# Kernel tuning notes

Measured on AMD Instinct MI355X. Metric: run time of the kernel, lower is better.

Reference implementation:

```python
import jax, jax.numpy as jnp
import numpy as np
import math

K = 8       # wavelet order (k)
C = 8       # channels (c)
ALPHA = 64  # retained Fourier modes
L = 0       # coarsest level
B = 32
N = 8192    # power of two


def setup_inputs() -> dict:
    key = jax.random.key(0)
    ks = jax.random.split(key, 14)
    ck = C * K
    scale = 1.0 / (ck * ck)  # matches torch: 1/(c*k)**2
    f32 = jnp.float32
    inp = {
        "x": jax.random.normal(ks[0], (B, N, C, K), dtype=f32),
        # SparseKernelFT1d weights (complex, stored as re/im): scale * rand
        "wA_re": scale * jax.random.uniform(ks[1], (ck, ck, ALPHA), dtype=f32),
        "wA_im": scale * jax.random.uniform(ks[2], (ck, ck, ALPHA), dtype=f32),
        "wB_re": scale * jax.random.uniform(ks[3], (ck, ck, ALPHA), dtype=f32),
        "wB_im": scale * jax.random.uniform(ks[4], (ck, ck, ALPHA), dtype=f32),
        "wC_re": scale * jax.random.uniform(ks[5], (ck, ck, ALPHA), dtype=f32),
        "wC_im": scale * jax.random.uniform(ks[6], (ck, ck, ALPHA), dtype=f32),
        # T0 linear layer (k -> k)
        "T0_w": jax.random.normal(ks[7], (K, K), dtype=f32) / math.sqrt(K),
        "T0_b": 0.01 * jax.random.normal(ks[8], (K,), dtype=f32),
        # Legendre wavelet filter buffers: ec_* are [H0.T;H1.T] / [G0.T;G1.T] (2k,k),
        # rc_* are [H0;G0] / [H1;G1] (2k,k). Stand-ins: random orthonormal-ish matrices
        # scaled like wavelet filters (same math regardless of exact values).
        "ec_s": jax.random.normal(ks[9], (2 * K, K), dtype=f32) / math.sqrt(2 * K),
        "ec_d": jax.random.normal(ks[10], (2 * K, K), dtype=f32) / math.sqrt(2 * K),
        "rc_e": jax.random.normal(ks[11], (2 * K, K), dtype=f32) / math.sqrt(2 * K),
        "rc_o": jax.random.normal(ks[12], (2 * K, K), dtype=f32) / math.sqrt(2 * K),
    }
    return inp


def _sparse_ft(x, w_re, w_im):
    # x: [B, N, c, k] -> spectral mixing over first ALPHA rfft modes
    Bb, Nn, c, k = x.shape
    xv = x.reshape(Bb, Nn, c * k).transpose(0, 2, 1)   # [B, ck, N]
    xf = jnp.fft.rfft(xv)                               # [B, ck, N//2+1] complex
    l = min(ALPHA, Nn // 2 + 1)
    W = (w_re[:, :, :l] + 1j * w_im[:, :, :l]).astype(jnp.complex64)
    of = jnp.einsum('bix,iox->box', xf[:, :, :l], W)
    out_ft = jnp.zeros((Bb, c * k, Nn // 2 + 1), dtype=jnp.complex64).at[:, :, :l].set(of)
    xo = jnp.fft.irfft(out_ft, n=Nn)                    # [B, ck, N] real
    return xo.transpose(0, 2, 1).reshape(Bb, Nn, c, k)


def reference(x, wA_re, wA_im, wB_re, wB_im, wC_re, wC_im, T0_w, T0_b,
              ec_s, ec_d, rc_e, rc_o):
    Bb, Nn, c, k = x.shape
    ns = int(math.floor(math.log2(Nn)))
    Ud, Us = [], []
    # --- decomposition ---
    for _ in range(ns - L):
        xa = jnp.concatenate([x[:, ::2], x[:, 1::2]], axis=-1)  # [B, N/2, c, 2k]
        d = xa @ ec_d                                           # [B, N/2, c, k]
        s = xa @ ec_s
        Ud.append(_sparse_ft(d, wA_re, wA_im) + _sparse_ft(s, wB_re, wB_im))
        Us.append(_sparse_ft(d, wC_re, wC_im))
        x = s
    # --- coarsest-level linear ---
    x = x @ T0_w.T + T0_b
    # --- reconstruction (u_s is None branch) ---
    for i in range(ns - 1 - L, -1, -1):
        x = x + Us[i]
        xc = jnp.concatenate([x, Ud[i]], axis=-1)               # [B, n, c, 2k]
        x_e = xc @ rc_e
        x_o = xc @ rc_o
        Bc, Nc, cc, _ = xc.shape
        x = jnp.stack([x_e, x_o], axis=2).reshape(Bc, Nc * 2, cc, K)  # interleave even/odd
    return (x,) + tuple(Ud) + tuple(Us)
```

## Files before the change

kernel.cpp:

```cpp
#include <hip/hip_runtime.h>

#define BB 32
#define CKD 64
#define CC 8
#define KK 8
#define FPW 132

__device__ const int D_FCB[14] = {0,8,12,14,15,16,17,18,19,20,21,22,23,24};
__device__ const int D_RP[14] = {0,32,48,56,60,62,63,64,65,66,67,68,69,70};
__device__ const int D_KBS[13] = {128,64,32,16,8,4,2,1,1,1,1,1,1};
__device__ const int D_PVP[13] = {0,128,192,224,240,248,252,254,255,256,257,258,259};
__device__ const int D_TB[14] = {0,64,96,112,120,124,126,127,128,129,130,131,132,133};
__device__ const int D_L[13]  = {64,64,64,64,64,64,33,17,9,5,3,2,1};
__device__ const int D_FTOF[13] = {0,524288,786432,917504,983040,1015808,1032192,
                                   1048576,1064960,1081344,1097728,1114112,1130496};
__device__ const int D_XP[65] = {0,13,25,36,46,56,65,74,83,92,100,108,116,124,132,140,
    148,156,163,170,177,184,191,198,205,212,219,226,233,240,247,254,261,268,274,280,
    286,292,298,304,310,316,322,328,334,340,346,352,358,364,370,376,382,388,394,400,
    406,412,418,424,430,436,442,448,454};

typedef __attribute__((ext_vector_type(4))) short s4v;
typedef __attribute__((ext_vector_type(8))) short s8v;
typedef __attribute__((ext_vector_type(4))) float f4v;

static __device__ __forceinline__ float4 ld4(const float* p){ return *(const float4*)p; }
static __device__ __forceinline__ size_t d_udo(int i){ return 33554432ull - (16777216u >> i); }
static __device__ __forceinline__ size_t d_uso(int i){ return 50329600ull - (16777216u >> i); }
static __device__ __forceinline__ size_t d_tof(int i){ return 128ull * (8192u - (8192u >> i)); }

static __device__ __forceinline__ unsigned short b16(float f) {
    unsigned u = __float_as_uint(f);
    u += 0x7FFFu + ((u >> 16) & 1u);
    return (unsigned short)(u >> 16);
}
static __device__ __forceinline__ float fb16(unsigned short h) {
    return __uint_as_float(((unsigned)h) << 16);
}

__global__ __launch_bounds__(256) void gen_tbl2_k(unsigned short* __restrict__ Th,
        unsigned short* __restrict__ Tl, unsigned short* __restrict__ Tfh,
        unsigned short* __restrict__ Tfl) {
    int lvl = blockIdx.y;
    int nh = 4096 >> lvl;
    int idx = blockIdx.x * 256 + threadIdx.x;
    if (blockIdx.z == 0) {
        if (idx >= nh * 128) return;
        int t = idx >> 7, k = idx & 127, x = k >> 1;
        int l = nh / 2 + 1; if (l > 64) l = 64;
        float v = 0.f;
        if (x < l) {
            int r = (x * t) & (nh - 1);
            float th = 6.283185307179586f * ((float)r / (float)nh);
            float s, c; sincosf(th, &s, &c);
            v = (k & 1) ? s : c;
        }
        unsigned short hi = b16(v);
        unsigned short lo = b16(v - fb16(hi));
        size_t off = d_tof(lvl) + idx;
        Th[off] = hi; Tl[off] = lo;
    } else {
        int nhp = nh < 128 ? 128 : nh;
        if (idx >= 128 * nhp) return;
        int j = idx & 7;
        int lane = (idx >> 3) & 63;
        int mt = (idx >> 9) & 7;
        int kb = idx >> 12;
        int row = mt*16 + (lane & 15);
        int t = kb*32 + (lane >> 4)*8 + j;
        int x = row >> 1;
        int l = nh / 2 + 1; if (l > 64) l = 64;
        float v = 0.f;
        if (x < l && t < nh) {
            int r = (x * t) & (nh - 1);
            float th = 6.283185307179586f * ((float)r / (float)nh);
            float s, c; sincosf(th, &s, &c);
            v = (row & 1) ? -s : c;
        }
        unsigned short hi = b16(v);
        unsigned short lo = b16(v - fb16(hi));
        size_t off = (size_t)D_FTOF[lvl] + idx;
        Tfh[off] = hi; Tfl[off] = lo;
    }
}

__global__ __launch_bounds__(256) void wtr_k(const float* __restrict__ wAr,
        const float* __restrict__ wAi, const float* __restrict__ wBr,
        const float* __restrict__ wBi, const float* __restrict__ wCr,
        const float* __restrict__ wCi, float* __restrict__ wt) {
    int x = blockIdx.x, arr = blockIdx.y;
    const float* W;
    switch (arr) {
        case 0: W = wAr; break;
        case 1: W = wAi; break;
        case 2: W = wBr; break;
        case 3: W = wBi; break;
        case 4: W = wCr; break;
        default: W = wCi; break;
    }
    float* o = wt + ((size_t)arr*64 + x)*4096;
    for (int q = threadIdx.x; q < 4096; q += 256)
        o[q] = W[(size_t)q*64 + x];
}

__global__ __launch_bounds__(256) void wbig_k(const float* __restrict__ wt,
        unsigned short* __restrict__ wbh, unsigned short* __restrict__ wbl) {
    int x = blockIdx.x;
    int f0 = blockIdx.y * 2048;
    for (int q = threadIdx.x; q < 2048; q += 256) {
        int f = f0 + q;
        int j = f & 7;
        int lane = (f >> 3) & 63;
        int nt = (f >> 9) & 15;
        int kt = f >> 13;
        int k = kt*32 + (lane >> 4)*8 + j;
        int n = nt*16 + (lane & 15);
        int pk = k >> 6, i = k & 63;
        int pn = n >> 6, o = n & 63;
        int arr; float sgn;
        switch ((pn << 2) | pk) {
            case 0:  arr = 0; sgn =  1.f; break;
            case 1:  arr = 1; sgn = -1.f; break;
            case 2:  arr = 2; sgn =  1.f; break;
            case 3:  arr = 3; sgn = -1.f; break;
            case 4:  arr = 1; sgn = -1.f; break;
            case 5:  arr = 0; sgn = -1.f; break;
            case 6:  arr = 3; sgn = -1.f; break;
            case 7:  arr = 2; sgn = -1.f; break;
            case 8:  arr = 4; sgn =  1.f; break;
            case 9:  arr = 5; sgn = -1.f; break;
            case 12: arr = 5; sgn = -1.f; break;
            case 13: arr = 4; sgn = -1.f; break;
            default: arr = -1; sgn = 0.f; break;
        }
        float v = 0.f;
        if (arr >= 0) v = sgn * wt[((size_t)arr*64 + x)*4096 + (size_t)i*64 + o];
        unsigned short h = b16(v);
        unsigned short l2 = b16(v - fb16(h));
        wbh[(size_t)x*65536 + f] = h;
        wbl[(size_t)x*65536 + f] = l2;
    }
}

__global__ __launch_bounds__(256) void decomp_k(const float* __restrict__ xin,
        const float* __restrict__ ecd, const float* __restrict__ ecs,
        float* __restrict__ dslot, float* __restrict__ sslot, int nh) {
    int idx = blockIdx.x * 256 + threadIdx.x;
    if (idx >= BB * nh * CC) return;
    int c = idx & 7;
    int t = (idx >> 3) % nh;
    int b = idx / (nh * CC);
    const float* p0 = xin + ((size_t)b * 2 * nh + 2 * t) * CKD + c * KK;
    float xa[16];
    float4 v;
    v = ld4(p0);      xa[0]=v.x; xa[1]=v.y; xa[2]=v.z; xa[3]=v.w;
    v = ld4(p0+4);    xa[4]=v.x; xa[5]=v.y; xa[6]=v.z; xa[7]=v.w;
    v = ld4(p0+64);   xa[8]=v.x; xa[9]=v.y; xa[10]=v.z; xa[11]=v.w;
    v = ld4(p0+68);   xa[12]=v.x; xa[13]=v.y; xa[14]=v.z; xa[15]=v.w;
    float dd[8], ss[8];
    #pragma unroll
    for (int m = 0; m < 8; m++) { dd[m] = 0.f; ss[m] = 0.f; }
    #pragma unroll
    for (int j = 0; j < 16; j++) {
        float xv = xa[j];
        #pragma unroll
        for (int m = 0; m < 8; m++) {
            dd[m] = fmaf(xv, ecd[j*8+m], dd[m]);
            ss[m] = fmaf(xv, ecs[j*8+m], ss[m]);
        }
    }
    size_t ob = ((size_t)b * nh + t) * CKD + c * KK;
    *(float4*)(dslot+ob)   = make_float4(dd[0],dd[1],dd[2],dd[3]);
    *(float4*)(dslot+ob+4) = make_float4(dd[4],dd[5],dd[6],dd[7]);
    *(float4*)(sslot+ob)   = make_float4(ss[0],ss[1],ss[2],ss[3]);
    *(float4*)(sslot+ob+4) = make_float4(ss[4],ss[5],ss[6],ss[7]);
}

__global__ __launch_bounds__(256) void decomp_small_k(const float* __restrict__ s4base,
        const float* __restrict__ ecd, const float* __restrict__ ecs,
        const float* __restrict__ T0w, const float* __restrict__ T0b,
        float* __restrict__ outbuf, float* __restrict__ xt0) {
    __shared__ float sA[128*64];
    __shared__ float sB[64*64];
    int b = blockIdx.x, tid = threadIdx.x;
    for (int lvl = 5; lvl <= 12; lvl++) {
        int nh = 4096 >> lvl;
        const float* src = (lvl == 5) ? (s4base + (size_t)b*256*CKD)
                                      : (((lvl - 6) & 1) ? sB : sA);
        float* dst = ((lvl - 5) & 1) ? sB : sA;
        float* dG = outbuf + d_udo(lvl) + (size_t)b*nh*CKD;
        float* sG = outbuf + d_uso(lvl) + (size_t)b*nh*CKD;
        for (int q = tid; q < nh*8; q += 256) {
            int c = q & 7, t = q >> 3;
            const float* p0 = src + (size_t)(2*t)*CKD + c*KK;
            float xa[16];
            float4 v;
            v = ld4(p0);      xa[0]=v.x; xa[1]=v.y; xa[2]=v.z; xa[3]=v.w;
            v = ld4(p0+4);    xa[4]=v.x; xa[5]=v.y; xa[6]=v.z; xa[7]=v.w;
            v = ld4(p0+64);   xa[8]=v.x; xa[9]=v.y; xa[10]=v.z; xa[11]=v.w;
            v = ld4(p0+68);   xa[12]=v.x; xa[13]=v.y; xa[14]=v.z; xa[15]=v.w;
            float dd[8], ss[8];
            #pragma unroll
            for (int m = 0; m < 8; m++) { dd[m] = 0.f; ss[m] = 0.f; }
            #pragma unroll
            for (int j = 0; j < 16; j++) {
                float xv = xa[j];
                #pragma unroll
                for (int m = 0; m < 8; m++) {
                    dd[m] = fmaf(xv, ecd[j*8+m], dd[m]);
                    ss[m] = fmaf(xv, ecs[j*8+m], ss[m]);
                }
            }
            size_t ob = (size_t)t * CKD + c * KK;
            *(float4*)(dG+ob)   = make_float4(dd[0],dd[1],dd[2],dd[3]);
            *(float4*)(dG+ob+4) = make_float4(dd[4],dd[5],dd[6],dd[7]);
            *(float4*)(sG+ob)   = make_float4(ss[0],ss[1],ss[2],ss[3]);
            *(float4*)(sG+ob+4) = make_float4(ss[4],ss[5],ss[6],ss[7]);
            float* dl = dst + t*CKD + c*KK;
            #pragma unroll
            for (int j = 0; j < 8; j++) dl[j] = ss[j];
        }
        __syncthreads();
    }
    if (tid < 64) {
        int m = tid & 7, c = tid >> 3;
        const float* xr = sB + c*KK;
        float a = T0b[m];
        #pragma unroll
        for (int j = 0; j < 8; j++) a = fmaf(xr[j], T0w[m*8+j], a);
        xt0[(size_t)b*64 + tid] = a;
    }
}

__global__ __launch_bounds__(256) void repack_k(const float* __restrict__ outbuf,
        unsigned* __restrict__ pv) {
    __shared__ unsigned vp[64*FPW];
    int slot = blockIdx.x;
    int lvl = 0;
    while (lvl < 12 && slot >= D_RP[lvl+1]) lvl++;
    int nh = 4096 >> lvl;
    int c = slot - D_RP[lvl];
    int t0s = c * 128;
    int kbs = D_KBS[lvl];
    int b = blockIdx.y, z = blockIdx.z;
    const float* V = outbuf + (z ? d_uso(lvl) : d_udo(lvl)) + (size_t)b * nh * CKD;
    int tid = threadIdx.x;
    #pragma unroll
    for (int q = 0; q < 8; q++) {
        int fi = tid + 256*q;
        int tl_ = fi >> 4;
        int t = t0s + tl_;
        int i4 = (fi & 15) * 4;
        float4 v = make_float4(0.f,0.f,0.f,0.f);
        if (t < nh) v = ld4(V + (size_t)t*CKD + i4);
        const float* pvv = &v.x;
        #pragma unroll
        for (int j = 0; j < 4; j++) {
            int row = i4 + j;
            float f = pvv[j];
            unsigned u = __float_as_uint(f);
            unsigned hi = u & 0xFFFF0000u;
            float r = f - __uint_as_float(hi);
            unsigned lo = __float_as_uint(r) & 0xFFFF0000u;
            int cw = tl_ ^ (((row >> 3) & 7) << 2);
            vp[row*FPW + cw] = (hi >> 16) | lo;
        }
    }
    __syncthreads();
    unsigned* P = pv + (size_t)D_PVP[lvl]*131072 + (size_t)b*kbs*4096;
    #pragma unroll
    for (int q = 0; q < 8; q++) {
        int fi = tid + 256*q;
        int j4 = fi & 1;
        int lane2 = (fi >> 1) & 63;
        int nt = (fi >> 7) & 3;
        int kbl = fi >> 9;
        int kbg = c*4 + kbl;
        if (kbg >= kbs) continue;
        int lrow = nt*16 + (lane2 & 15);
        int cb = kbl*32 + (lane2 >> 4)*8 + j4*4;
        int rsw = ((lrow >> 3) & 7) << 2;
        uint4 v = *(const uint4*)&vp[lrow*FPW + (cb ^ rsw)];
        *(uint4*)(P + (((size_t)(kbg*8 + z*4 + nt))*64 + lane2)*8 + j4*4) = v;
    }
}

__global__ __launch_bounds__(256) void fft_fwd_mfma_k(const unsigned* __restrict__ pv,
        const unsigned short* __restrict__ Tfh, const unsigned short* __restrict__ Tfl,
        float* __restrict__ xfpf, float2* __restrict__ xf_all) {
    int slot = blockIdx.x;
    int lvl = 0;
    while (lvl < 12 && slot >= D_FCB[lvl+1]) lvl++;
    int kbs = D_KBS[lvl];
    int nslots = D_FCB[lvl+1] - D_FCB[lvl];
    int kb0 = (slot - D_FCB[lvl]) * 16;
    int kb1 = kb0 + 16; if (kb1 > kbs) kb1 = kbs;
    int b = blockIdx.y;
    const unsigned* PV = pv + (size_t)D_PVP[lvl]*131072 + (size_t)b*kbs*4096;
    const unsigned short* THb = Tfh + D_FTOF[lvl];
    const unsigned short* TLb = Tfl + D_FTOF[lvl];
    int tid = threadIdx.x;
    int w = tid >> 6, lane = tid & 63;
    int col = lane & 15, khi = lane >> 4;
    int mt0 = w * 2;
    f4v acc[2][8];
    #pragma unroll
    for (int m = 0; m < 2; m++)
        #pragma unroll
        for (int n = 0; n < 8; n++) acc[m][n] = (f4v){0.f,0.f,0.f,0.f};
    for (int kb = kb0; kb < kb1; kb++) {
        s8v ah[2], al[2];
        #pragma unroll
        for (int m = 0; m < 2; m++) {
            size_t fo = (((size_t)kb*8 + (mt0 + m))*64 + lane)*8;
            ah[m] = *(const s8v*)(THb + fo);
            al[m] = *(const s8v*)(TLb + fo);
        }
        #pragma unroll
        for (int n = 0; n < 8; n++) {
            const unsigned* bp = PV + (((size_t)(kb*8 + n))*64 + lane)*8;
            uint4 w0 = *(const uint4*)bp;
            uint4 w1 = *(const uint4*)(bp + 4);
            s8v bh, bl;
            const unsigned* pw = &w0.x;
            #pragma unroll
            for (int j = 0; j < 4; j++) {
                bh[j] = (short)(pw[j] & 0xFFFFu);
                bl[j] = (short)(pw[j] >> 16);
            }
            pw = &w1.x;
            #pragma unroll
            for (int j = 0; j < 4; j++) {
                bh[4+j] = (short)(pw[j] & 0xFFFFu);
                bl[4+j] = (short)(pw[j] >> 16);
            }
            #pragma unroll
            for (int m = 0; m < 2; m++) {
                acc[m][n] = __builtin_amdgcn_mfma_f32_16x16x32_bf16(ah[m], bh, acc[m][n], 0,0,0);
                acc[m][n] = __builtin_amdgcn_mfma_f32_16x16x32_bf16(ah[m], bl, acc[m][n], 0,0,0);
                acc[m][n] = __builtin_amdgcn_mfma_f32_16x16x32_bf16(al[m], bh, acc[m][n], 0,0,0);
            }
        }
    }
    if (nslots == 1) {
        float* XB = (float*)xf_all + (size_t)lvl*524288 + (size_t)b*16384;
        #pragma unroll
        for (int m = 0; m < 2; m++) {
            int m0 = (mt0 + m)*16 + khi*4;
            #pragma unroll
            for (int n = 0; n < 8; n++) {
                int ic = n*16 + col;
                int z = ic >> 6, i = ic & 63;
                float* X = XB + (size_t)z*8192;
                #pragma unroll
                for (int r = 0; r < 4; r++) {
                    int row = m0 + r;
                    X[(((size_t)(row >> 1)*64 + i) << 1) | (row & 1)] = acc[m][n][r];
                }
            }
        }
    } else {
        #pragma unroll
        for (int m = 0; m < 2; m++) {
            int m0 = (mt0 + m)*16 + khi*4;
            #pragma unroll
            for (int n = 0; n < 8; n++) {
                int ic = n*16 + col;
                int z = ic >> 6, i = ic & 63;
                float* P = xfpf + ((size_t)slot*64 + (size_t)b*2 + z) * 8192;
                #pragma unroll
                for (int r = 0; r < 4; r++)
                    P[(size_t)(m0 + r)*64 + i] = acc[m][n][r];
            }
        }
    }
}

__global__ __launch_bounds__(256) void reduce_fwd_k(const float* __restrict__ xfpf,
        float2* __restrict__ xf_all) {
    int lvl = blockIdx.y;
    int e = blockIdx.x * 256 + threadIdx.x;
    int j = e & 4095;
    int bz = e >> 12;
    int x = j >> 6, i = j & 63;
    int c0 = D_FCB[lvl], c1 = D_FCB[lvl+1];
    float re = 0.f, im = 0.f;
    for (int c = c0; c < c1; c++) {
        size_t base = ((size_t)c*64 + bz) * 8192;
        re += xfpf[base + (size_t)(2*x)*64 + i];
        im += xfpf[base + (size_t)(2*x+1)*64 + i];
    }
    xf_all[(size_t)lvl*262144 + (size_t)bz*4096 + j] = make_float2(re, im);
}

__global__ __launch_bounds__(256) void mix_mfma_k(const float2* __restrict__ xf_all,
        const unsigned short* __restrict__ wbh, const unsigned short* __restrict__ wbl,
        unsigned* __restrict__ ofp) {
    __shared__ unsigned ax[32*260];
    int x = 0;
    while (x < 64 && (int)blockIdx.x >= D_XP[x+1]) x++;
    int lvl = blockIdx.x - D_XP[x];
    int nh = 4096 >> lvl;
    const float2* xfL = xf_all + (size_t)lvl*262144;
    int tid = threadIdx.x;
    for (int q = tid; q < 4096; q += 256) {
        int b = q >> 7, z = (q >> 6) & 1, i = q & 63;
        float2 v = xfL[((size_t)b*2 + z)*4096 + (size_t)x*64 + i];
        int sw = ((b >> 3) & 7) << 2;
        int kR = z*128 + i;
        unsigned uR = __float_as_uint(v.x);
        unsigned hiR = uR & 0xFFFF0000u;
        float rR = v.x - __uint_as_float(hiR);
        unsigned loR = __float_as_uint(rR) & 0xFFFF0000u;
        ax[b*260 + (kR ^ sw)] = (hiR >> 16) | loR;
        unsigned uI = __float_as_uint(v.y);
        unsigned hiI = uI & 0xFFFF0000u;
        float rI = v.y - __uint_as_float(hiI);
        unsigned loI = __float_as_uint(rI) & 0xFFFF0000u;
        ax[b*260 + ((kR + 64) ^ sw)] = (hiI >> 16) | loI;
    }
    __syncthreads();
    int w4 = tid >> 6, lane = tid & 63;
    int col = lane & 15, khi = lane >> 4;
    int mt = w4 & 1, nt0 = (w4 >> 1) * 8;
    int arow = mt*16 + col;
    int asw = ((arow >> 3) & 7) << 2;
    const unsigned* ap = ax + arow*260;
    const unsigned short* WBH = wbh + (size_t)x*65536;
    const unsigned short* WBL = wbl + (size_t)x*65536;
    f4v acc[8];
    #pragma unroll
    for (int n = 0; n < 8; n++) acc[n] = (f4v){0.f,0.f,0.f,0.f};
    #pragma unroll
    for (int kt = 0; kt < 8; kt++) {
        int cb = kt*32 + khi*8;
        uint4 a0 = *(const uint4*)(ap + (cb ^ asw));
        uint4 a1 = *(const uint4*)(ap + ((cb + 4) ^ asw));
        s8v ah, al;
        const unsigned* pw = &a0.x;
        #pragma unroll
        for (int j = 0; j < 4; j++) {
            ah[j] = (short)(pw[j] & 0xFFFFu);
            al[j] = (short)(pw[j] >> 16);
        }
        pw = &a1.x;
        #pragma unroll
        for (int j = 0; j < 4; j++) {
            ah[4+j] = (short)(pw[j] & 0xFFFFu);
            al[4+j] = (short)(pw[j] >> 16);
        }
        #pragma unroll
        for (int n = 0; n < 8; n++) {
            int nt = nt0 + n;
            size_t fo = (((size_t)kt*16 + nt)*64 + lane)*8;
            s8v bh = *(const s8v*)(WBH + fo);
            s8v bl = *(const s8v*)(WBL + fo);
            acc[n] = __builtin_amdgcn_mfma_f32_16x16x32_bf16(ah, bh, acc[n], 0, 0, 0);
            acc[n] = __builtin_amdgcn_mfma_f32_16x16x32_bf16(ah, bl, acc[n], 0, 0, 0);
            acc[n] = __builtin_amdgcn_mfma_f32_16x16x32_bf16(al, bh, acc[n], 0, 0, 0);
        }
    }
    float wfac = (x == 0 || 2*x == nh) ? 1.f : 2.f;
    float sc = wfac / (float)nh;
    int k0 = 2*x;
    #pragma unroll
    for (int n = 0; n < 8; n++) {
        int nn = nt0 + n;
        int pn = nn >> 2;
        int o = (nn & 3)*16 + col;
        int z = pn >> 1;
        int kr = k0 + (pn & 1);
        #pragma unroll
        for (int r = 0; r < 4; r++) {
            int b = mt*16 + khi*4 + r;
            size_t base = (((size_t)lvl*32 + b)*2 + z)*8192 + (size_t)kr*64 + o;
            float v = sc * acc[n][r];
            unsigned short h = b16(v);
            unsigned short l2 = b16(v - fb16(h));
            ofp[base] = (unsigned)h | ((unsigned)l2 << 16);
        }
    }
}

__global__ __launch_bounds__(256) void fft_inv_mfma_k(
        const unsigned* __restrict__ ofp,
        const unsigned short* __restrict__ Th,  const unsigned short* __restrict__ Tl,
        float* __restrict__ outbuf) {
    __shared__ unsigned gp[2*64*132];
    int lvl = 0;
    while (lvl < 12 && (int)blockIdx.x >= D_TB[lvl+1]) lvl++;
    int g = blockIdx.x - D_TB[lvl];
    int nh = 4096 >> lvl;
    int tbase = g * 64;
    int b = blockIdx.y;
    int tid = threadIdx.x;
    const unsigned* Gp = ofp + (((size_t)lvl*32 + b)*2)*8192;
    #pragma unroll
    for (int q = 0; q < 16; q++) {
        int fi = tid + 256*q;
        int z = fi >> 11;
        int rem = fi & 2047;
        int k = rem >> 4, o4 = (rem & 15)*4;
        uint4 v = *(const uint4*)(Gp + (size_t)z*8192 + (size_t)k*64 + o4);
        const unsigned* pw = &v.x;
        #pragma unroll
        for (int i = 0; i < 4; i++)
            gp[z*8448 + (o4+i)*132 + k] = pw[i];
    }
    __syncthreads();
    int w = tid >> 6;
    int lane = tid & 63;
    int tb = tbase + w*16;
    if (tb >= nh) return;
    int trow = lane & 15, khi = lane >> 4;
    int tA = tb + trow; if (tA >= nh) tA = nh - 1;
    const unsigned short* THp = Th + d_tof(lvl) + (size_t)tA*128 + khi*8;
    const unsigned short* TLp = Tl + d_tof(lvl) + (size_t)tA*128 + khi*8;
    f4v acc[8];
    #pragma unroll
    for (int n = 0; n < 8; n++) acc[n] = (f4v){0.f,0.f,0.f,0.f};
    #pragma unroll
    for (int kk = 0; kk < 4; kk++) {
        s8v ah = *(const s8v*)(THp + kk*32);
        s8v al = *(const s8v*)(TLp + kk*32);
        #pragma unroll
        for (int n = 0; n < 8; n++) {
            int z = n >> 2;
            int off = z*8448 + ((n & 3)*16 + trow)*132 + kk*32 + khi*8;
            uint4 w0 = *(const uint4*)(gp + off);
            uint4 w1 = *(const uint4*)(gp + off + 4);
            s8v bh, bl;
            const unsigned* pw = &w0.x;
            #pragma unroll
            for (int j = 0; j < 4; j++) {
                bh[j] = (short)(pw[j] & 0xFFFFu);
                bl[j] = (short)(pw[j] >> 16);
            }
            pw = &w1.x;
            #pragma unroll
            for (int j = 0; j < 4; j++) {
                bh[4+j] = (short)(pw[j] & 0xFFFFu);
                bl[4+j] = (short)(pw[j] >> 16);
            }
            acc[n] = __builtin_amdgcn_mfma_f32_16x16x32_bf16(ah, bh, acc[n], 0, 0, 0);
            acc[n] = __builtin_amdgcn_mfma_f32_16x16x32_bf16(ah, bl, acc[n], 0, 0, 0);
            acc[n] = __builtin_amdgcn_mfma_f32_16x16x32_bf16(al, bh, acc[n], 0, 0, 0);
        }
    }
    float* U0 = outbuf + d_udo(lvl) + (size_t)b * nh * CKD;
    float* U1 = outbuf + d_uso(lvl) + (size_t)b * nh * CKD;
    int thi4 = khi * 4;
    #pragma unroll
    for (int n = 0; n < 8; n++) {
        float* U = (n >> 2) ? U1 : U0;
        int ocol = (n & 3)*16 + trow;
        #pragma unroll
        for (int r = 0; r < 4; r++) {
            int t = tb + thi4 + r;
            if (t < nh) U[(size_t)t*64 + ocol] = acc[n][r];
        }
    }
}

__global__ __launch_bounds__(256) void recon_small_k(const float* __restrict__ xt0,
        const float* __restrict__ outbuf,
        const float* __restrict__ rce, const float* __restrict__ rco,
        float* __restrict__ rb0) {
    __shared__ float xA[128*64];
    __shared__ float xB[64*64];
    int b = blockIdx.x, tid = threadIdx.x;
    if (tid < 64) xB[tid] = xt0[(size_t)b*64 + tid];
    __syncthreads();
    for (int i = 12; i >= 6; i--) {
        int nh = 4096 >> i;
        const float* cur = ((i == 12) || !(i & 1)) ? xB : xA;
        float* nxt = (i & 1) ? xB : xA;
        const float* Us = outbuf + d_uso(i) + (size_t)b*nh*CKD;
        const float* Ud = outbuf + d_udo(i) + (size_t)b*nh*CKD;
        for (int q = tid; q < nh*8; q += 256) {
            int c = q & 7, t = q >> 3;
            size_t base = (size_t)t*CKD + c*KK;
            float xc[16];
            float4 a0 = ld4(cur+base), a1 = ld4(cur+base+4);
            float4 u0 = ld4(Us+base),  u1 = ld4(Us+base+4);
            float4 d0 = ld4(Ud+base),  d1 = ld4(Ud+base+4);
            xc[0]=a0.x+u0.x; xc[1]=a0.y+u0.y; xc[2]=a0.z+u0.z; xc[3]=a0.w+u0.w;
            xc[4]=a1.x+u1.x; xc[5]=a1.y+u1.y; xc[6]=a1.z+u1.z; xc[7]=a1.w+u1.w;
            xc[8]=d0.x;  xc[9]=d0.y;  xc[10]=d0.z; xc[11]=d0.w;
            xc[12]=d1.x; xc[13]=d1.y; xc[14]=d1.z; xc[15]=d1.w;
            float e[8], o2[8];
            #pragma unroll
            for (int m = 0; m < 8; m++) { e[m] = 0.f; o2[m] = 0.f; }
            #pragma unroll
            for (int j = 0; j < 16; j++) {
                float xv = xc[j];
                #pragma unroll
                for (int m = 0; m < 8; m++) {
                    e[m]  = fmaf(xv, rce[j*8+m], e[m]);
                    o2[m] = fmaf(xv, rco[j*8+m], o2[m]);
                }
            }
            if (i > 6) {
                float* pe = nxt + (size_t)(2*t)*CKD + c*KK;
                #pragma unroll
                for (int j = 0; j < 8; j++) { pe[j] = e[j]; pe[CKD + j] = o2[j]; }
            } else {
                float* pe = rb0 + ((size_t)b*128 + 2*t)*CKD + c*KK;
                *(float4*)(pe)      = make_float4(e[0],e[1],e[2],e[3]);
                *(float4*)(pe+4)    = make_float4(e[4],e[5],e[6],e[7]);
                *(float4*)(pe+64)   = make_float4(o2[0],o2[1],o2[2],o2[3]);
                *(float4*)(pe+68)   = make_float4(o2[4],o2[5],o2[6],o2[7]);
            }
        }
        __syncthreads();
    }
}

__global__ __launch_bounds__(256) void recon_k(const float* __restrict__ xin,
        const float* __restrict__ us, const float* __restrict__ ud,
        const float* __restrict__ rce, const float* __restrict__ rco,
        float* __restrict__ xout, int nh) {
    int idx = blockIdx.x*256 + threadIdx.x;
    if (idx >= BB*nh*CC) return;
    int c = idx & 7;
    int t = (idx >> 3) % nh;
    int b = idx / (nh*CC);
    size_t base = ((size_t)b*nh + t)*CKD + c*KK;
    float xc[16];
    float4 a0 = ld4(xin+base), a1 = ld4(xin+base+4);
    float4 u0 = ld4(us+base),  u1 = ld4(us+base+4);
    float4 d0 = ld4(ud+base),  d1 = ld4(ud+base+4);
    xc[0]=a0.x+u0.x; xc[1]=a0.y+u0.y; xc[2]=a0.z+u0.z; xc[3]=a0.w+u0.w;
    xc[4]=a1.x+u1.x; xc[5]=a1.y+u1.y; xc[6]=a1.z+u1.z; xc[7]=a1.w+u1.w;
    xc[8]=d0.x;  xc[9]=d0.y;  xc[10]=d0.z; xc[11]=d0.w;
    xc[12]=d1.x; xc[13]=d1.y; xc[14]=d1.z; xc[15]=d1.w;
    float e[8], o2[8];
    #pragma unroll
    for (int m = 0; m < 8; m++) { e[m] = 0.f; o2[m] = 0.f; }
    #pragma unroll
    for (int j = 0; j < 16; j++) {
        float xv = xc[j];
        #pragma unroll
        for (int m = 0; m < 8; m++) {
            e[m]  = fmaf(xv, rce[j*8+m], e[m]);
            o2[m] = fmaf(xv, rco[j*8+m], o2[m]);
        }
    }
    size_t ob = ((size_t)b*2*nh + 2*t)*CKD + c*KK;
    *(float4*)(xout+ob)      = make_float4(e[0],e[1],e[2],e[3]);
    *(float4*)(xout+ob+4)    = make_float4(e[4],e[5],e[6],e[7]);
    *(float4*)(xout+ob+64)   = make_float4(o2[0],o2[1],o2[2],o2[3]);
    *(float4*)(xout+ob+68)   = make_float4(o2[4],o2[5],o2[6],o2[7]);
}

extern "C" void kernel_launch(void* const* d_in, const int* in_sizes, int n_in,
                              void* d_out, int out_size, void* d_ws, size_t ws_size,
                              hipStream_t stream) {
    const float* x   = (const float*)d_in[0];
    const float* wAr = (const float*)d_in[1];
    const float* wAi = (const float*)d_in[2];
    const float* wBr = (const float*)d_in[3];
    const float* wBi = (const float*)d_in[4];
    const float* wCr = (const float*)d_in[5];
    const float* wCi = (const float*)d_in[6];
    const float* T0w = (const float*)d_in[7];
    const float* T0b = (const float*)d_in[8];
    const float* ecs = (const float*)d_in[9];
    const float* ecd = (const float*)d_in[10];
    const float* rce = (const float*)d_in[11];
    const float* rco = (const float*)d_in[12];
    float* out = (float*)d_out;
    float* wsf = (float*)d_ws;

    size_t p = 0;
    float2* xf_all = (float2*)(wsf + p); p += 6815744;
    unsigned* ofp = (unsigned*)(wsf + p); p += 6815744;
    unsigned short* Th  = (unsigned short*)(wsf + p); p += 528384;
    unsigned short* Tl  = (unsigned short*)(wsf + p); p += 528384;
    unsigned short* Tfh = (unsigned short*)(wsf + p); p += 573440;
    unsigned short* Tfl = (unsigned short*)(wsf + p); p += 573440;
    float*  wt   = wsf + p; p += 1572864;
    unsigned short* wbh = (unsigned short*)(wsf + p); p += 2097152;
    unsigned short* wbl = (unsigned short*)(wsf + p); p += 2097152;
    float*  xt0  = wsf + p; p += 2048;
    float*  rb0  = wsf + p; p += 4194304;
    float*  rb1  = wsf + p; p += 8388608;
    float*  xfpf = wsf + p; p += 36700160;
    unsigned* pv = (unsigned*)(wsf + p); p += 34078720;
    (void)ws_size; (void)in_sizes; (void)n_in; (void)out_size;

    size_t udo[13], uso[13];
    for (int i = 0; i < 13; i++) {
        udo[i] = 33554432ull - (16777216u >> i);
        uso[i] = 50329600ull - (16777216u >> i);
    }

    gen_tbl2_k<<<dim3(2048, 13, 2), 256, 0, stream>>>(Th, Tl, Tfh, Tfl);
    wtr_k<<<dim3(64, 6), 256, 0, stream>>>(wAr, wAi, wBr, wBi, wCr, wCi, wt);
    wbig_k<<<dim3(64, 32), 256, 0, stream>>>(wt, wbh, wbl);

    for (int i = 0; i < 5; i++) {
        int nh = 4096 >> i;
        const float* xin_l = (i == 0) ? x : (out + uso[i-1]);
        int tot = BB * nh * CC;
        decomp_k<<<(tot + 255)/256, 256, 0, stream>>>(xin_l, ecd, ecs, out + udo[i], out + uso[i], nh);
    }
    decomp_small_k<<<BB, 256, 0, stream>>>(out + uso[4], ecd, ecs, T0w, T0b, out, xt0);

    repack_k<<<dim3(70, BB, 2), 256, 0, stream>>>(out, pv);
    fft_fwd_mfma_k<<<dim3(24, BB), 256, 0, stream>>>(pv, Tfh, Tfl, xfpf, xf_all);
    reduce_fwd_k<<<dim3(1024, 3), 256, 0, stream>>>(xfpf, xf_all);
    mix_mfma_k<<<454, 256, 0, stream>>>(xf_all, wbh, wbl, ofp);
    fft_inv_mfma_k<<<dim3(133, BB), 256, 0, stream>>>(ofp, Th, Tl, out);

    recon_small_k<<<BB, 256, 0, stream>>>(xt0, out, rce, rco, rb0);
    const float* rin = rb0;
    for (int i = 5; i >= 0; i--) {
        int nh = 4096 >> i;
        float* ro = (i == 0) ? out : ((i & 1) ? rb1 : rb0);
        int tot = BB * nh * CC;
        recon_k<<<(tot + 255)/256, 256, 0, stream>>>(rin, out + uso[i], out + udo[i], rce, rco, ro, nh);
        rin = ro;
    }
}
```

Before: 438.6 us.

## Fuse repack into decomposition and drop split-K forward FFT reduction

```diff
diff --git a/kernel.cpp b/kernel.cpp
--- a/kernel.cpp
+++ b/kernel.cpp
@@ -6,12 +6,9 @@
 #define KK 8
 #define FPW 132
 
-__device__ const int D_FCB[14] = {0,8,12,14,15,16,17,18,19,20,21,22,23,24};
-__device__ const int D_RP[14] = {0,32,48,56,60,62,63,64,65,66,67,68,69,70};
 __device__ const int D_KBS[13] = {128,64,32,16,8,4,2,1,1,1,1,1,1};
 __device__ const int D_PVP[13] = {0,128,192,224,240,248,252,254,255,256,257,258,259};
 __device__ const int D_TB[14] = {0,64,96,112,120,124,126,127,128,129,130,131,132,133};
-__device__ const int D_L[13]  = {64,64,64,64,64,64,33,17,9,5,3,2,1};
 __device__ const int D_FTOF[13] = {0,524288,786432,917504,983040,1015808,1032192,
                                    1048576,1064960,1081344,1097728,1114112,1130496};
 __device__ const int D_XP[65] = {0,13,25,36,46,56,65,74,83,92,100,108,116,124,132,140,
@@ -35,6 +32,13 @@
 }
 static __device__ __forceinline__ float fb16(unsigned short h) {
     return __uint_as_float(((unsigned)h) << 16);
+}
+static __device__ __forceinline__ unsigned packhl(float f) {
+    unsigned u = __float_as_uint(f);
+    unsigned hi = u & 0xFFFF0000u;
+    float r = f - __uint_as_float(hi);
+    unsigned lo = __float_as_uint(r) & 0xFFFF0000u;
+    return (hi >> 16) | lo;
 }
 
 __global__ __launch_bounds__(256) void gen_tbl2_k(unsigned short* __restrict__ Th,
@@ -143,52 +147,82 @@
 
 __global__ __launch_bounds__(256) void decomp_k(const float* __restrict__ xin,
         const float* __restrict__ ecd, const float* __restrict__ ecs,
-        float* __restrict__ dslot, float* __restrict__ sslot, int nh) {
-    int idx = blockIdx.x * 256 + threadIdx.x;
-    if (idx >= BB * nh * CC) return;
-    int c = idx & 7;
-    int t = (idx >> 3) % nh;
-    int b = idx / (nh * CC);
-    const float* p0 = xin + ((size_t)b * 2 * nh + 2 * t) * CKD + c * KK;
-    float xa[16];
-    float4 v;
-    v = ld4(p0);      xa[0]=v.x; xa[1]=v.y; xa[2]=v.z; xa[3]=v.w;
-    v = ld4(p0+4);    xa[4]=v.x; xa[5]=v.y; xa[6]=v.z; xa[7]=v.w;
-    v = ld4(p0+64);   xa[8]=v.x; xa[9]=v.y; xa[10]=v.z; xa[11]=v.w;
-    v = ld4(p0+68);   xa[12]=v.x; xa[13]=v.y; xa[14]=v.z; xa[15]=v.w;
-    float dd[8], ss[8];
-    #pragma unroll
-    for (int m = 0; m < 8; m++) { dd[m] = 0.f; ss[m] = 0.f; }
-    #pragma unroll
-    for (int j = 0; j < 16; j++) {
-        float xv = xa[j];
-        #pragma unroll
-        for (int m = 0; m < 8; m++) {
-            dd[m] = fmaf(xv, ecd[j*8+m], dd[m]);
-            ss[m] = fmaf(xv, ecs[j*8+m], ss[m]);
-        }
-    }
-    size_t ob = ((size_t)b * nh + t) * CKD + c * KK;
-    *(float4*)(dslot+ob)   = make_float4(dd[0],dd[1],dd[2],dd[3]);
-    *(float4*)(dslot+ob+4) = make_float4(dd[4],dd[5],dd[6],dd[7]);
-    *(float4*)(sslot+ob)   = make_float4(ss[0],ss[1],ss[2],ss[3]);
-    *(float4*)(sslot+ob+4) = make_float4(ss[4],ss[5],ss[6],ss[7]);
+        float* __restrict__ sslot, unsigned* __restrict__ pvL,
+        int nh, int kbs) {
+    __shared__ unsigned vd[64*FPW];
+    __shared__ unsigned vs[64*FPW];
+    int chunk = blockIdx.x, b = blockIdx.y;
+    int t0 = chunk * 128;
+    int tid = threadIdx.x;
+    #pragma unroll
+    for (int wi = 0; wi < 4; wi++) {
+        int q = tid + wi*256;
+        int c = q & 7, tl = q >> 3;
+        int t = t0 + tl;
+        const float* p0 = xin + ((size_t)b*2*nh + 2*t)*CKD + c*KK;
+        float xa[16];
+        float4 v;
+        v = ld4(p0);      xa[0]=v.x; xa[1]=v.y; xa[2]=v.z; xa[3]=v.w;
+        v = ld4(p0+4);    xa[4]=v.x; xa[5]=v.y; xa[6]=v.z; xa[7]=v.w;
+        v = ld4(p0+64);   xa[8]=v.x; xa[9]=v.y; xa[10]=v.z; xa[11]=v.w;
+        v = ld4(p0+68);   xa[12]=v.x; xa[13]=v.y; xa[14]=v.z; xa[15]=v.w;
+        float dd[8], ss[8];
+        #pragma unroll
+        for (int m = 0; m < 8; m++) { dd[m] = 0.f; ss[m] = 0.f; }
+        #pragma unroll
+        for (int j = 0; j < 16; j++) {
+            float xv = xa[j];
+            #pragma unroll
+            for (int m = 0; m < 8; m++) {
+                dd[m] = fmaf(xv, ecd[j*8+m], dd[m]);
+                ss[m] = fmaf(xv, ecs[j*8+m], ss[m]);
+            }
+        }
+        float* sp = sslot + ((size_t)b*nh + t)*CKD + c*KK;
+        *(float4*)sp     = make_float4(ss[0],ss[1],ss[2],ss[3]);
+        *(float4*)(sp+4) = make_float4(ss[4],ss[5],ss[6],ss[7]);
+        #pragma unroll
+        for (int j = 0; j < 8; j++) {
+            int row = c*8 + j;
+            int cw = tl ^ (((row >> 3) & 7) << 2);
+            vd[row*FPW + cw] = packhl(dd[j]);
+            vs[row*FPW + cw] = packhl(ss[j]);
+        }
+    }
+    __syncthreads();
+    unsigned* P = pvL + (size_t)b*kbs*4096;
+    #pragma unroll
+    for (int qq = 0; qq < 16; qq++) {
+        int fi = tid + 256*qq;
+        int z = fi >> 11;
+        int rem = fi & 2047;
+        int j4 = rem & 1;
+        int lane2 = (rem >> 1) & 63;
+        int nt = (rem >> 7) & 3;
+        int kbl = rem >> 9;
+        int kbg = chunk*4 + kbl;
+        int lrow = nt*16 + (lane2 & 15);
+        int cb = kbl*32 + (lane2 >> 4)*8 + j4*4;
+        int rsw = ((lrow >> 3) & 7) << 2;
+        const unsigned* src = z ? vs : vd;
+        uint4 v = *(const uint4*)&src[lrow*FPW + (cb ^ rsw)];
+        *(uint4*)(P + (((size_t)(kbg*8 + z*4 + nt))*64 + lane2)*8 + j4*4) = v;
+    }
 }
 
 __global__ __launch_bounds__(256) void decomp_small_k(const float* __restrict__ s4base,
         const float* __restrict__ ecd, const float* __restrict__ ecs,
         const float* __restrict__ T0w, const float* __restrict__ T0b,
-        float* __restrict__ outbuf, float* __restrict__ xt0) {
+        unsigned* __restrict__ pv, float* __restrict__ xt0) {
     __shared__ float sA[128*64];
     __shared__ float sB[64*64];
+    __shared__ unsigned sDp[128*64];
     int b = blockIdx.x, tid = threadIdx.x;
     for (int lvl = 5; lvl <= 12; lvl++) {
         int nh = 4096 >> lvl;
         const float* src = (lvl == 5) ? (s4base + (size_t)b*256*CKD)
                                       : (((lvl - 6) & 1) ? sB : sA);
         float* dst = ((lvl - 5) & 1) ? sB : sA;
-        float* dG = outbuf + d_udo(lvl) + (size_t)b*nh*CKD;
-        float* sG = outbuf + d_uso(lvl) + (size_t)b*nh*CKD;
         for (int q = tid; q < nh*8; q += 256) {
             int c = q & 7, t = q >> 3;
             const float* p0 = src + (size_t)(2*t)*CKD + c*KK;
@@ -210,14 +244,33 @@
                     ss[m] = fmaf(xv, ecs[j*8+m], ss[m]);
                 }
             }
-            size_t ob = (size_t)t * CKD + c * KK;
-            *(float4*)(dG+ob)   = make_float4(dd[0],dd[1],dd[2],dd[3]);
-            *(float4*)(dG+ob+4) = make_float4(dd[4],dd[5],dd[6],dd[7]);
-            *(float4*)(sG+ob)   = make_float4(ss[0],ss[1],ss[2],ss[3]);
-            *(float4*)(sG+ob+4) = make_float4(ss[4],ss[5],ss[6],ss[7]);
             float* dl = dst + t*CKD + c*KK;
-            #pragma unroll
-            for (int j = 0; j < 8; j++) dl[j] = ss[j];
+            unsigned* dp = sDp + t*CKD + c*KK;
+            #pragma unroll
+            for (int j = 0; j < 8; j++) {
+                dl[j] = ss[j];
+                dp[j] = packhl(dd[j]);
+            }
+        }
+        __syncthreads();
+        int kbs = D_KBS[lvl];
+        unsigned* P = pv + (size_t)D_PVP[lvl]*131072 + (size_t)b*kbs*4096;
+        for (int f = tid; f < kbs*512; f += 256) {
+            int lane = f & 63;
+            int zn = (f >> 6) & 7;
+            int kb = f >> 9;
+            int z = zn >> 2, nt = zn & 3;
+            int i = nt*16 + (lane & 15);
+            int tb2 = kb*32 + (lane >> 4)*8;
+            unsigned vals[8];
+            #pragma unroll
+            for (int j = 0; j < 8; j++) {
+                int t = tb2 + j;
+                vals[j] = z ? packhl(dst[t*CKD + i]) : sDp[t*CKD + i];
+            }
+            unsigned* pp = P + (((size_t)(kb*8 + z*4 + nt))*64 + lane)*8;
+            *(uint4*)pp     = make_uint4(vals[0],vals[1],vals[2],vals[3]);
+            *(uint4*)(pp+4) = make_uint4(vals[4],vals[5],vals[6],vals[7]);
         }
         __syncthreads();
     }
@@ -231,69 +284,11 @@
     }
 }
 
-__global__ __launch_bounds__(256) void repack_k(const float* __restrict__ outbuf,
-        unsigned* __restrict__ pv) {
-    __shared__ unsigned vp[64*FPW];
-    int slot = blockIdx.x;
-    int lvl = 0;
-    while (lvl < 12 && slot >= D_RP[lvl+1]) lvl++;
-    int nh = 4096 >> lvl;
-    int c = slot - D_RP[lvl];
-    int t0s = c * 128;
-    int kbs = D_KBS[lvl];
-    int b = blockIdx.y, z = blockIdx.z;
-    const float* V = outbuf + (z ? d_uso(lvl) : d_udo(lvl)) + (size_t)b * nh * CKD;
-    int tid = threadIdx.x;
-    #pragma unroll
-    for (int q = 0; q < 8; q++) {
-        int fi = tid + 256*q;
-        int tl_ = fi >> 4;
-        int t = t0s + tl_;
-        int i4 = (fi & 15) * 4;
-        float4 v = make_float4(0.f,0.f,0.f,0.f);
-        if (t < nh) v = ld4(V + (size_t)t*CKD + i4);
-        const float* pvv = &v.x;
-        #pragma unroll
-        for (int j = 0; j < 4; j++) {
-            int row = i4 + j;
-            float f = pvv[j];
-            unsigned u = __float_as_uint(f);
-            unsigned hi = u & 0xFFFF0000u;
-            float r = f - __uint_as_float(hi);
-            unsigned lo = __float_as_uint(r) & 0xFFFF0000u;
-            int cw = tl_ ^ (((row >> 3) & 7) << 2);
-            vp[row*FPW + cw] = (hi >> 16) | lo;
-        }
-    }
-    __syncthreads();
-    unsigned* P = pv + (size_t)D_PVP[lvl]*131072 + (size_t)b*kbs*4096;
-    #pragma unroll
-    for (int q = 0; q < 8; q++) {
-        int fi = tid + 256*q;
-        int j4 = fi & 1;
-        int lane2 = (fi >> 1) & 63;
-        int nt = (fi >> 7) & 3;
-        int kbl = fi >> 9;
-        int kbg = c*4 + kbl;
-        if (kbg >= kbs) continue;
-        int lrow = nt*16 + (lane2 & 15);
-        int cb = kbl*32 + (lane2 >> 4)*8 + j4*4;
-        int rsw = ((lrow >> 3) & 7) << 2;
-        uint4 v = *(const uint4*)&vp[lrow*FPW + (cb ^ rsw)];
-        *(uint4*)(P + (((size_t)(kbg*8 + z*4 + nt))*64 + lane2)*8 + j4*4) = v;
-    }
-}
-
 __global__ __launch_bounds__(256) void fft_fwd_mfma_k(const unsigned* __restrict__ pv,
         const unsigned short* __restrict__ Tfh, const unsigned short* __restrict__ Tfl,
-        float* __restrict__ xfpf, float2* __restrict__ xf_all) {
-    int slot = blockIdx.x;
-    int lvl = 0;
-    while (lvl < 12 && slot >= D_FCB[lvl+1]) lvl++;
+        float2* __restrict__ xf_all) {
+    int lvl = blockIdx.x;
     int kbs = D_KBS[lvl];
-    int nslots = D_FCB[lvl+1] - D_FCB[lvl];
-    int kb0 = (slot - D_FCB[lvl]) * 16;
-    int kb1 = kb0 + 16; if (kb1 > kbs) kb1 = kbs;
     int b = blockIdx.y;
     const unsigned* PV = pv + (size_t)D_PVP[lvl]*131072 + (size_t)b*kbs*4096;
     const unsigned short* THb = Tfh + D_FTOF[lvl];
@@ -307,7 +302,7 @@
     for (int m = 0; m < 2; m++)
         #pragma unroll
         for (int n = 0; n < 8; n++) acc[m][n] = (f4v){0.f,0.f,0.f,0.f};
-    for (int kb = kb0; kb < kb1; kb++) {
+    for (int kb = 0; kb < kbs; kb++) {
         s8v ah[2], al[2];
         #pragma unroll
         for (int m = 0; m < 2; m++) {
@@ -341,55 +336,22 @@
             }
         }
     }
-    if (nslots == 1) {
-        float* XB = (float*)xf_all + (size_t)lvl*524288 + (size_t)b*16384;
-        #pragma unroll
-        for (int m = 0; m < 2; m++) {
-            int m0 = (mt0 + m)*16 + khi*4;
-            #pragma unroll
-            for (int n = 0; n < 8; n++) {
-                int ic = n*16 + col;
-                int z = ic >> 6, i = ic & 63;
-                float* X = XB + (size_t)z*8192;
-                #pragma unroll
-                for (int r = 0; r < 4; r++) {
-                    int row = m0 + r;
-                    X[(((size_t)(row >> 1)*64 + i) << 1) | (row & 1)] = acc[m][n][r];
-                }
-            }
-        }
-    } else {
-        #pragma unroll
-        for (int m = 0; m < 2; m++) {
-            int m0 = (mt0 + m)*16 + khi*4;
-            #pragma unroll
-            for (int n = 0; n < 8; n++) {
-                int ic = n*16 + col;
-                int z = ic >> 6, i = ic & 63;
-                float* P = xfpf + ((size_t)slot*64 + (size_t)b*2 + z) * 8192;
-                #pragma unroll
-                for (int r = 0; r < 4; r++)
-                    P[(size_t)(m0 + r)*64 + i] = acc[m][n][r];
-            }
-        }
-    }
-}
-
-__global__ __launch_bounds__(256) void reduce_fwd_k(const float* __restrict__ xfpf,
-        float2* __restrict__ xf_all) {
-    int lvl = blockIdx.y;
-    int e = blockIdx.x * 256 + threadIdx.x;
-    int j = e & 4095;
-    int bz = e >> 12;
-    int x = j >> 6, i = j & 63;
-    int c0 = D_FCB[lvl], c1 = D_FCB[lvl+1];
-    float re = 0.f, im = 0.f;
-    for (int c = c0; c < c1; c++) {
-        size_t base = ((size_t)c*64 + bz) * 8192;
-        re += xfpf[base + (size_t)(2*x)*64 + i];
-        im += xfpf[base + (size_t)(2*x+1)*64 + i];
-    }
-    xf_all[(size_t)lvl*262144 + (size_t)bz*4096 + j] = make_float2(re, im);
+    float* XB = (float*)xf_all + (size_t)lvl*524288 + (size_t)b*16384;
+    #pragma unroll
+    for (int m = 0; m < 2; m++) {
+        int m0 = (mt0 + m)*16 + khi*4;
+        #pragma unroll
+        for (int n = 0; n < 8; n++) {
+            int ic = n*16 + col;
+            int z = ic >> 6, i = ic & 63;
+            float* X = XB + (size_t)z*8192;
+            #pragma unroll
+            for (int r = 0; r < 4; r++) {
+                int row = m0 + r;
+                X[(((size_t)(row >> 1)*64 + i) << 1) | (row & 1)] = acc[m][n][r];
+            }
+        }
+    }
 }
 
 __global__ __launch_bounds__(256) void mix_mfma_k(const float2* __restrict__ xf_all,
@@ -407,16 +369,8 @@
         float2 v = xfL[((size_t)b*2 + z)*4096 + (size_t)x*64 + i];
         int sw = ((b >> 3) & 7) << 2;
         int kR = z*128 + i;
-        unsigned uR = __float_as_uint(v.x);
-        unsigned hiR = uR & 0xFFFF0000u;
-        float rR = v.x - __uint_as_float(hiR);
-        unsigned loR = __float_as_uint(rR) & 0xFFFF0000u;
-        ax[b*260 + (kR ^ sw)] = (hiR >> 16) | loR;
-        unsigned uI = __float_as_uint(v.y);
-        unsigned hiI = uI & 0xFFFF0000u;
-        float rI = v.y - __uint_as_float(hiI);
-        unsigned loI = __float_as_uint(rI) & 0xFFFF0000u;
-        ax[b*260 + ((kR + 64) ^ sw)] = (hiI >> 16) | loI;
+        ax[b*260 + (kR ^ sw)] = packhl(v.x);
+        ax[b*260 + ((kR + 64) ^ sw)] = packhl(v.y);
     }
     __syncthreads();
     int w4 = tid >> 6, lane = tid & 63;
@@ -473,10 +427,7 @@
         for (int r = 0; r < 4; r++) {
             int b = mt*16 + khi*4 + r;
             size_t base = (((size_t)lvl*32 + b)*2 + z)*8192 + (size_t)kr*64 + o;
-            float v = sc * acc[n][r];
-            unsigned short h = b16(v);
-            unsigned short l2 = b16(v - fb16(h));
-            ofp[base] = (unsigned)h | ((unsigned)l2 << 16);
+            ofp[base] = packhl(sc * acc[n][r]);
         }
     }
 }
@@ -684,7 +635,6 @@
     float*  xt0  = wsf + p; p += 2048;
     float*  rb0  = wsf + p; p += 4194304;
     float*  rb1  = wsf + p; p += 8388608;
-    float*  xfpf = wsf + p; p += 36700160;
     unsigned* pv = (unsigned*)(wsf + p); p += 34078720;
     (void)ws_size; (void)in_sizes; (void)n_in; (void)out_size;
 
@@ -693,6 +643,8 @@
         udo[i] = 33554432ull - (16777216u >> i);
         uso[i] = 50329600ull - (16777216u >> i);
     }
+    const int kbs_h[5] = {128,64,32,16,8};
+    const int pvp_h[5] = {0,128,192,224,240};
 
     gen_tbl2_k<<<dim3(2048, 13, 2), 256, 0, stream>>>(Th, Tl, Tfh, Tfl);
     wtr_k<<<dim3(64, 6), 256, 0, stream>>>(wAr, wAi, wBr, wBi, wCr, wCi, wt);
@@ -701,14 +653,12 @@
     for (int i = 0; i < 5; i++) {
         int nh = 4096 >> i;
         const float* xin_l = (i == 0) ? x : (out + uso[i-1]);
-        int tot = BB * nh * CC;
-        decomp_k<<<(tot + 255)/256, 256, 0, stream>>>(xin_l, ecd, ecs, out + udo[i], out + uso[i], nh);
-    }
-    decomp_small_k<<<BB, 256, 0, stream>>>(out + uso[4], ecd, ecs, T0w, T0b, out, xt0);
-
-    repack_k<<<dim3(70, BB, 2), 256, 0, stream>>>(out, pv);
-    fft_fwd_mfma_k<<<dim3(24, BB), 256, 0, stream>>>(pv, Tfh, Tfl, xfpf, xf_all);
-    reduce_fwd_k<<<dim3(1024, 3), 256, 0, stream>>>(xfpf, xf_all);
+        decomp_k<<<dim3(nh/128, BB), 256, 0, stream>>>(xin_l, ecd, ecs,
+                out + uso[i], pv + (size_t)pvp_h[i]*131072, nh, kbs_h[i]);
+    }
+    decomp_small_k<<<BB, 256, 0, stream>>>(out + uso[4], ecd, ecs, T0w, T0b, pv, xt0);
+
+    fft_fwd_mfma_k<<<dim3(13, BB), 256, 0, stream>>>(pv, Tfh, Tfl, xf_all);
     mix_mfma_k<<<454, 256, 0, stream>>>(xf_all, wbh, wbl, ofp);
     fft_inv_mfma_k<<<dim3(133, BB), 256, 0, stream>>>(ofp, Th, Tl, out);
 
```

New measurement: 625.4 us. 42.6% more time.
